# Optimization experiments

Measured on AMD Instinct MI355X. Metric: run time of the kernel, lower is better.

Reference implementation:

```python
import jax, jax.numpy as jnp
from jax import lax
import numpy as np

B, NQ, NT = 32, 256, 512
INF = jnp.float32(1e30)  # stand-in for float('inf') mask fill; all targets are valid here
W_TRANS, W_QPOS, W_ROT = 1.0, 1.0, 1.0


def setup_inputs() -> dict:
    key = jax.random.key(0)
    k1, k2, k3, k4 = jax.random.split(key, 4)
    rot = jax.random.normal(k3, (B, NQ, 4), jnp.float32)
    rot = rot / jnp.linalg.norm(rot, axis=-1, keepdims=True)  # unit quaternions
    return {
        "translation_norm": jax.random.normal(k1, (B, NQ, 3), jnp.float32),
        "qpos_norm": jax.random.normal(k2, (B, NQ, 16), jnp.float32),
        "rotation": rot,
        "norm_pose": jax.random.normal(k4, (B, NT, 23), jnp.float32),
    }


def _l1_cost(p, t):
    # p: [B, NQ, D], t: [B, NT, D] -> [B, NQ, NT] pairwise L1
    return jnp.abs(p[:, :, None, :] - t[:, None, :, :]).sum(-1)


def _final_cost(translation_norm, qpos_norm, rotation, norm_pose):
    valid = jnp.abs(norm_pose).sum(-1) > 0  # [B, NT]
    cost = (W_TRANS * _l1_cost(translation_norm, norm_pose[..., :3])
            + W_QPOS * _l1_cost(qpos_norm, norm_pose[..., 3:19])
            + W_ROT * (1.0 - jnp.abs(jnp.einsum('bqd,bnd->bqn', rotation, norm_pose[..., 19:]))))
    return jnp.where(valid[:, None, :], cost, INF)


def _hungarian(cost):
    """Rectangular LSAP via Jonker-Volgenant shortest augmenting path
    (same algorithm as scipy.optimize.linear_sum_assignment).
    cost: [n, m] with n <= m. Returns col4row [n]: matched column per row."""
    n, m = cost.shape

    def solve_row(carry, cur_row):
        u, v, col4row, row4col = carry

        # --- Dijkstra-like search for the shortest augmenting path ---
        def s_cond(st):
            return st[6] < 0  # until a free column (sink) is found

        def s_body(st):
            i, minVal, SR, SC, spc, path, _sink = st
            SR = SR.at[i].set(True)
            r = minVal + cost[i] - u[i] - v          # reduced costs for row i
            upd = (~SC) & (r < spc)
            spc = jnp.where(upd, r, spc)
            path = jnp.where(upd, i, path)
            masked = jnp.where(SC, INF, spc)
            j = jnp.argmin(masked).astype(jnp.int32)
            minVal = masked[j]
            SC = SC.at[j].set(True)
            free = row4col[j] < 0
            sink = jnp.where(free, j, jnp.int32(-1))
            i = jnp.where(free, i, row4col[j])
            return (i, minVal, SR, SC, spc, path, sink)

        st0 = (cur_row, jnp.float32(0.0),
               jnp.zeros((n,), bool), jnp.zeros((m,), bool),
               jnp.full((m,), INF), jnp.full((m,), -1, jnp.int32), jnp.int32(-1))
        _i, minVal, SR, SC, spc, path, sink = lax.while_loop(s_cond, s_body, st0)

        # --- dual variable updates ---
        spc_row = spc[jnp.clip(col4row, 0, m - 1)]  # [n]; invalid rows masked by SR
        du = jnp.where(jnp.arange(n) == cur_row, minVal, minVal - spc_row)
        u = u + jnp.where(SR, du, 0.0)
        v = v - jnp.where(SC, minVal - spc, 0.0)

        # --- augment along the alternating path back to cur_row ---
        def a_cond(st):
            return ~st[3]

        def a_body(st):
            j, c4r, r4c, _done = st
            i = path[j]
            r4c = r4c.at[j].set(i)
            nj = c4r[i]
            c4r = c4r.at[i].set(j)
            return (nj, c4r, r4c, i == cur_row)

        _, col4row, row4col, _ = lax.while_loop(
            a_cond, a_body, (sink, col4row, row4col, False))
        return (u, v, col4row, row4col), None

    carry0 = (jnp.zeros((n,), jnp.float32), jnp.zeros((m,), jnp.float32),
              jnp.full((n,), -1, jnp.int32), jnp.full((m,), -1, jnp.int32))
    (u, v, col4row, row4col), _ = lax.scan(
        solve_row, carry0, jnp.arange(n, dtype=jnp.int32))
    return col4row


def reference(translation_norm, qpos_norm, rotation, norm_pose):
    final_cost = _final_cost(translation_norm, qpos_norm, rotation, norm_pose)
    # batched Hungarian (replaces per-batch scipy linear_sum_assignment loop)
    per_query_gt_inds = jax.vmap(_hungarian)(final_cost)        # [B, NQ]
    query_matched_mask = jnp.ones_like(per_query_gt_inds)        # all matched (NT >= NQ)
    return final_cost, per_query_gt_inds, query_matched_mask
```

## Files before the change

kernel.cpp:

```cpp
#include <hip/hip_runtime.h>

constexpr int kB  = 32;
constexpr int kNQ = 256;
constexpr int kNT = 512;
constexpr float kInf = 1e30f;
constexpr int kQTile = 32;
constexpr int kSlots = 48;

__global__ __launch_bounds__(512)
void cost_kernel(const float* __restrict__ trans,
                 const float* __restrict__ qpos,
                 const float* __restrict__ rot,
                 const float* __restrict__ pose,
                 float* __restrict__ cost)
{
    __shared__ float sPose[kNT * 23];

    const int b     = blockIdx.x;
    const int qBase = blockIdx.y * kQTile;
    const int tid   = threadIdx.x;

    const float* pb = pose + (size_t)b * kNT * 23;
    for (int idx = tid; idx < kNT * 23; idx += 512) sPose[idx] = pb[idx];
    __syncthreads();

    float T[23];
    #pragma unroll
    for (int d = 0; d < 23; ++d) T[d] = sPose[tid * 23 + d];

    float s = 0.f;
    #pragma unroll
    for (int d = 0; d < 23; ++d) s += fabsf(T[d]);
    const bool valid = (s > 0.f);

    const float* tr = trans + ((size_t)b * kNQ + qBase) * 3;
    const float* qp = qpos  + ((size_t)b * kNQ + qBase) * 16;
    const float* rt = rot   + ((size_t)b * kNQ + qBase) * 4;
    float* cb = cost + ((size_t)b * kNQ + qBase) * kNT + tid;

    for (int q = 0; q < kQTile; ++q) {
        const float Q0 = tr[q * 3 + 0], Q1 = tr[q * 3 + 1], Q2 = tr[q * 3 + 2];
        float a = fabsf(Q0 - T[0]);
        a += fabsf(Q1 - T[1]);
        a += fabsf(Q2 - T[2]);
        float bsum = 0.f;
        #pragma unroll
        for (int d = 0; d < 16; ++d) bsum += fabsf(qp[q * 16 + d] - T[3 + d]);
        const float r0 = rt[q * 4 + 0], r1 = rt[q * 4 + 1];
        const float r2 = rt[q * 4 + 2], r3 = rt[q * 4 + 3];
        float dot = r0 * T[19] + r1 * T[20] + r2 * T[21] + r3 * T[22];
        float c = (a + bsum) + (1.0f - fabsf(dot));
        cb[(size_t)q * kNT] = valid ? c : kInf;
    }
}

__device__ __forceinline__ unsigned wave_min_u32(unsigned x) {
    unsigned t;
    t = (unsigned)__builtin_amdgcn_update_dpp((int)0xFFFFFFFF, (int)x, 0x111, 0xF, 0xF, false); x = t < x ? t : x;
    t = (unsigned)__builtin_amdgcn_update_dpp((int)0xFFFFFFFF, (int)x, 0x112, 0xF, 0xF, false); x = t < x ? t : x;
    t = (unsigned)__builtin_amdgcn_update_dpp((int)0xFFFFFFFF, (int)x, 0x114, 0xF, 0xF, false); x = t < x ? t : x;
    t = (unsigned)__builtin_amdgcn_update_dpp((int)0xFFFFFFFF, (int)x, 0x118, 0xF, 0xF, false); x = t < x ? t : x;
    t = (unsigned)__builtin_amdgcn_update_dpp((int)0xFFFFFFFF, (int)x, 0x142, 0xF, 0xF, false); x = t < x ? t : x;
    t = (unsigned)__builtin_amdgcn_update_dpp((int)0xFFFFFFFF, (int)x, 0x143, 0xF, 0xF, false); x = t < x ? t : x;
    return (unsigned)__builtin_amdgcn_readlane((int)x, 63);
}

__global__ __launch_bounds__(256)
void hungarian_kernel(const float* __restrict__ cost,
                      float* __restrict__ outInds,
                      float* __restrict__ outMask)
{
    __shared__ float rowCache[kSlots * kNT];
    __shared__ float u[kNQ];
    __shared__ int   col4row[kNQ];
    __shared__ int   row4col[kNT];
    __shared__ int   colBest[kNT];
    __shared__ int   pathL[kNT];
    __shared__ int   rowArg[kNQ];

    const int b   = blockIdx.x;
    const int tid = threadIdx.x;
    const float* __restrict__ C = cost + (size_t)b * kNQ * kNT;

    {
        const float4* Crow = (const float4*)(C + (size_t)tid * kNT);
        float bm = kInf; int barg = 0;
        #pragma unroll 4
        for (int j4 = 0; j4 < kNT / 4; ++j4) {
            float4 cc = Crow[j4];
            const int jb = j4 * 4;
            if (cc.x < bm) { bm = cc.x; barg = jb + 0; }
            if (cc.y < bm) { bm = cc.y; barg = jb + 1; }
            if (cc.z < bm) { bm = cc.z; barg = jb + 2; }
            if (cc.w < bm) { bm = cc.w; barg = jb + 3; }
        }
        u[tid]      = bm;
        rowArg[tid] = barg;
        col4row[tid] = -1;
    }
    row4col[tid] = -1;         row4col[tid + 256] = -1;
    colBest[tid] = 0x7fffffff; colBest[tid + 256] = 0x7fffffff;
    __syncthreads();
    atomicMin(&colBest[rowArg[tid]], tid);
    __syncthreads();
    {
        const int j = rowArg[tid];
        if (colBest[j] == tid) { col4row[tid] = j; row4col[j] = tid; }
    }
    __syncthreads();

    if (tid < 64) {
        const int lane = tid;
        float vR[8];
        #pragma unroll
        for (int c = 0; c < 8; ++c) vR[c] = 0.f;

        int tagReg = -1;
        int rr     = 0;

        for (int cur = 0; cur < kNQ; ++cur) {
            if (col4row[cur] >= 0) continue;

            float spcR[8]; int pathR[8];
            #pragma unroll
            for (int c = 0; c < 8; ++c) { spcR[c] = kInf; pathR[c] = -1; }
            unsigned scMask = 0;

            int   i      = cur;
            float minVal = 0.f;
            int   sink   = -1;

            for (int guard = 0; guard < kNT + 2 && sink < 0; ++guard) {
                const float ui = u[i];
                float4 p0, p1;
                const unsigned long long hm = __ballot(tagReg == i);
                if (hm != 0ull) {
                    const int slot = (int)__ffsll(hm) - 1;
                    const float4* lp = (const float4*)&rowCache[slot * kNT + lane * 8];
                    p0 = lp[0]; p1 = lp[1];
                } else {
                    const float4* rp = (const float4*)(C + (size_t)i * kNT + lane * 8);
                    p0 = rp[0]; p1 = rp[1];
                    if (guard != 0) {
                        float4* wp = (float4*)&rowCache[rr * kNT + lane * 8];
                        wp[0] = p0; wp[1] = p1;
                        if (lane == rr) tagReg = i;
                        rr = rr + 1; if (rr == kSlots) rr = 0;
                    }
                }
                const float cc[8] = {p0.x, p0.y, p0.z, p0.w, p1.x, p1.y, p1.z, p1.w};
                #pragma unroll
                for (int c = 0; c < 8; ++c) {
                    if (!((scMask >> c) & 1u)) {
                        const float r = ((minVal + cc[c]) - ui) - vR[c];
                        if (r < spcR[c]) { spcR[c] = r; pathR[c] = i; }
                    }
                }

                unsigned sp[8];
                #pragma unroll
                for (int c = 0; c < 8; ++c)
                    sp[c] = ((scMask >> c) & 1u) ? 0xFFFFFFFFu
                                                 : __float_as_uint(spcR[c]);
                unsigned mA = sp[1] < sp[0] ? sp[1] : sp[0]; int aA = sp[1] < sp[0] ? 1 : 0;
                unsigned mB = sp[3] < sp[2] ? sp[3] : sp[2]; int aB = sp[3] < sp[2] ? 3 : 2;
                unsigned mC = sp[5] < sp[4] ? sp[5] : sp[4]; int aC = sp[5] < sp[4] ? 5 : 4;
                unsigned mD = sp[7] < sp[6] ? sp[7] : sp[6]; int aD = sp[7] < sp[6] ? 7 : 6;
                unsigned mAB = mB < mA ? mB : mA; int aAB = mB < mA ? aB : aA;
                unsigned mCD = mD < mC ? mD : mC; int aCD = mD < mC ? aD : aC;
                unsigned lvu = mCD < mAB ? mCD : mAB; int lc = mCD < mAB ? aCD : aAB;
                const int lix  = lane * 8 + lc;
                const int spec = row4col[lix];

                const unsigned gmu = wave_min_u32(lvu);
                const unsigned long long bal = __ballot(lvu == gmu);
                const int wl    = (int)__ffsll((unsigned long long)bal) - 1;
                const int jstar = __builtin_amdgcn_readlane(lix, wl);
                const int own   = __builtin_amdgcn_readlane(spec, wl);
                minVal = __uint_as_float(gmu);

                if (wl == lane) scMask |= 1u << (jstar & 7);
                if (own < 0) sink = jstar;
                else         i    = own;
            }

            if (lane == 0) u[cur] += minVal;
            #pragma unroll
            for (int c = 0; c < 8; ++c) {
                if ((scMask >> c) & 1u) {
                    const int j = lane * 8 + c;
                    const int r = row4col[j];
                    const float d = minVal - spcR[c];
                    if (r >= 0) u[r] += d;
                    vR[c] -= d;
                    pathL[j] = pathR[c];
                }
            }
            __threadfence_block();

            if (lane == 0 && sink >= 0) {
                int j = sink;
                while (true) {
                    const int pi = pathL[j];
                    row4col[j] = pi;
                    const int nj = col4row[pi];
                    col4row[pi] = j;
                    if (pi == cur) break;
                    j = nj;
                }
            }
            __threadfence_block();
        }
    }
    __syncthreads();

    outInds[(size_t)b * kNQ + tid] = (float)col4row[tid];
    outMask[(size_t)b * kNQ + tid] = 1.0f;
}

extern "C" void kernel_launch(void* const* d_in, const int* in_sizes, int n_in,
                              void* d_out, int out_size, void* d_ws, size_t ws_size,
                              hipStream_t stream) {
    const float* trans = (const float*)d_in[0];
    const float* qpos  = (const float*)d_in[1];
    const float* rot   = (const float*)d_in[2];
    const float* pose  = (const float*)d_in[3];

    float* out  = (float*)d_out;
    float* cost = out;
    float* inds = out + (size_t)kB * kNQ * kNT;
    float* mask = inds + (size_t)kB * kNQ;

    dim3 g1(kB, kNQ / kQTile);
    cost_kernel<<<g1, 512, 0, stream>>>(trans, qpos, rot, pose, cost);
    hungarian_kernel<<<kB, 256, 0, stream>>>(cost, inds, mask);
}
```

Before: 521.7 us.

## Enlarge row cache, use strided LDS layout, coalesce initial row-min scan

The LDS row cache grows from 48 to 64 slots, and cached rows are now stored with a stride-64 layout so each lane reads and writes conflict-free scalar words instead of float4 pairs. The initial per-row minimum scan now uses one wave per row, with coalesced loads and a DPP wave-min over order-preserving float keys, in place of one thread serially scanning a whole row. The aim is more cache hits in the serial augmenting-path loop, fewer LDS bank conflicts, and faster initialisation. In exchange it uses more shared memory (64×512 floats, 128 KB for the cache alone) and issues eight LDS ops per access instead of two.

```diff
diff --git a/kernel.cpp b/kernel.cpp
--- a/kernel.cpp
+++ b/kernel.cpp
@@ -5,7 +5,7 @@
 constexpr int kNT = 512;
 constexpr float kInf = 1e30f;
 constexpr int kQTile = 32;
-constexpr int kSlots = 48;
+constexpr int kSlots = 64;
 
 __global__ __launch_bounds__(512)
 void cost_kernel(const float* __restrict__ trans,
@@ -65,6 +65,15 @@
     return (unsigned)__builtin_amdgcn_readlane((int)x, 63);
 }
 
+__device__ __forceinline__ unsigned fkey(float f) {
+    unsigned s = __float_as_uint(f);
+    return (s & 0x80000000u) ? ~s : (s | 0x80000000u);
+}
+__device__ __forceinline__ float funkey(unsigned k) {
+    unsigned s = (k & 0x80000000u) ? (k & 0x7fffffffu) : ~k;
+    return __uint_as_float(s);
+}
+
 __global__ __launch_bounds__(256)
 void hungarian_kernel(const float* __restrict__ cost,
                       float* __restrict__ outInds,
@@ -83,21 +92,26 @@
     const float* __restrict__ C = cost + (size_t)b * kNQ * kNT;
 
     {
-        const float4* Crow = (const float4*)(C + (size_t)tid * kNT);
-        float bm = kInf; int barg = 0;
-        #pragma unroll 4
-        for (int j4 = 0; j4 < kNT / 4; ++j4) {
-            float4 cc = Crow[j4];
-            const int jb = j4 * 4;
-            if (cc.x < bm) { bm = cc.x; barg = jb + 0; }
-            if (cc.y < bm) { bm = cc.y; barg = jb + 1; }
-            if (cc.z < bm) { bm = cc.z; barg = jb + 2; }
-            if (cc.w < bm) { bm = cc.w; barg = jb + 3; }
+        const int wv = tid >> 6, ln = tid & 63;
+        for (int r = 0; r < 64; ++r) {
+            const int row = wv * 64 + r;
+            const float4* rp = (const float4*)(C + (size_t)row * kNT + ln * 8);
+            const float4 a0 = rp[0], a1 = rp[1];
+            const float cc[8] = {a0.x, a0.y, a0.z, a0.w, a1.x, a1.y, a1.z, a1.w};
+            unsigned bv = 0xFFFFFFFFu; int bc = 0;
+            #pragma unroll
+            for (int c = 0; c < 8; ++c) {
+                const unsigned k = fkey(cc[c]);
+                if (k < bv) { bv = k; bc = c; }
+            }
+            const unsigned g = wave_min_u32(bv);
+            const unsigned long long bal = __ballot(bv == g);
+            const int wl  = (int)__ffsll(bal) - 1;
+            const int jmn = __builtin_amdgcn_readlane(ln * 8 + bc, wl);
+            if (ln == 0) { u[row] = funkey(g); rowArg[row] = jmn; }
         }
-        u[tid]      = bm;
-        rowArg[tid] = barg;
-        col4row[tid] = -1;
-    }
+    }
+    col4row[tid] = -1;
     row4col[tid] = -1;         row4col[tid + 256] = -1;
     colBest[tid] = 0x7fffffff; colBest[tid + 256] = 0x7fffffff;
     __syncthreads();
@@ -132,23 +146,26 @@
 
             for (int guard = 0; guard < kNT + 2 && sink < 0; ++guard) {
                 const float ui = u[i];
-                float4 p0, p1;
+                float cc[8];
                 const unsigned long long hm = __ballot(tagReg == i);
                 if (hm != 0ull) {
                     const int slot = (int)__ffsll(hm) - 1;
-                    const float4* lp = (const float4*)&rowCache[slot * kNT + lane * 8];
-                    p0 = lp[0]; p1 = lp[1];
+                    const float* lp = &rowCache[slot * kNT + lane];
+                    #pragma unroll
+                    for (int c = 0; c < 8; ++c) cc[c] = lp[c * 64];
                 } else {
                     const float4* rp = (const float4*)(C + (size_t)i * kNT + lane * 8);
-                    p0 = rp[0]; p1 = rp[1];
+                    const float4 p0 = rp[0], p1 = rp[1];
+                    cc[0]=p0.x; cc[1]=p0.y; cc[2]=p0.z; cc[3]=p0.w;
+                    cc[4]=p1.x; cc[5]=p1.y; cc[6]=p1.z; cc[7]=p1.w;
                     if (guard != 0) {
-                        float4* wp = (float4*)&rowCache[rr * kNT + lane * 8];
-                        wp[0] = p0; wp[1] = p1;
+                        float* wp = &rowCache[rr * kNT + lane];
+                        #pragma unroll
+                        for (int c = 0; c < 8; ++c) wp[c * 64] = cc[c];
                         if (lane == rr) tagReg = i;
                         rr = rr + 1; if (rr == kSlots) rr = 0;
                     }
                 }
-                const float cc[8] = {p0.x, p0.y, p0.z, p0.w, p1.x, p1.y, p1.z, p1.w};
                 #pragma unroll
                 for (int c = 0; c < 8; ++c) {
                     if (!((scMask >> c) & 1u)) {
@@ -174,7 +191,7 @@
 
                 const unsigned gmu = wave_min_u32(lvu);
                 const unsigned long long bal = __ballot(lvu == gmu);
-                const int wl    = (int)__ffsll((unsigned long long)bal) - 1;
+                const int wl    = (int)__ffsll(bal) - 1;
                 const int jstar = __builtin_amdgcn_readlane(lix, wl);
                 const int own   = __builtin_amdgcn_readlane(spec, wl);
                 minVal = __uint_as_float(gmu);
```

Measured after the change: 533.6 us. 1.02x slower.
